# Kernel optimization log

Measured on AMD Instinct MI355X. Metric: run time of the kernel, lower is better.

The kernel has to match this reference:

```python
import jax, jax.numpy as jnp
import numpy as np

H = 128  # hidden_dim
F = 64   # node_feat_dim


def setup_inputs() -> dict:
    key = jax.random.key(0)
    ks = jax.random.split(key, 24)
    N, E, NR, NT = 50000, 400000, 20000, 20000
    inp = {
        "mol_x": jax.random.normal(ks[0], (N, F), jnp.float32),
        "pos": jax.random.normal(ks[1], (N, 3), jnp.float32),
        "reaction_x": jax.random.normal(ks[2], (NR, F), jnp.float32),
        "target_x": jax.random.normal(ks[3], (NT, F), jnp.float32),
        "edge_index": jax.random.randint(ks[4], (2, E), 0, N, jnp.int32),
    }
    def lin(k, fan_in, fan_out):
        s = 1.0 / np.sqrt(fan_in)
        kw, kb = jax.random.split(k)
        W = jax.random.uniform(kw, (fan_in, fan_out), jnp.float32, -s, s)
        b = jax.random.uniform(kb, (fan_out,), jnp.float32, -s, s)
        return W, b
    inp["W_node"], inp["b_node"] = lin(ks[5], F, H)
    inp["W_att1"], inp["b_att1"] = lin(ks[6], 2 * H + 3, H)
    inp["W_att2"], inp["b_att2"] = lin(ks[7], H, 1)
    inp["W_upd"], inp["b_upd"] = lin(ks[8], H, H)
    inp["Wy1"], inp["by1"] = lin(ks[9], H, 64)
    inp["Wy2"], inp["by2"] = lin(ks[10], 64, 1)
    inp["Wa1"], inp["ba1"] = lin(ks[11], H, 64)
    inp["Wa2"], inp["ba2"] = lin(ks[12], 64, 1)
    return inp


def reference(mol_x, pos, reaction_x, target_x, edge_index,
              W_node, b_node, W_att1, b_att1, W_att2, b_att2,
              W_upd, b_upd, Wy1, by1, Wy2, by2, Wa1, ba1, Wa2, ba2):
    N = mol_x.shape[0]
    # node encoder
    h = mol_x @ W_node + b_node                      # [N, H]
    src, dst = edge_index[0], edge_index[1]          # PyG: x_j = source, x_i = target
    x_j = h[src]                                      # [E, H]
    x_i = h[dst]                                      # [E, H]
    dist = pos[dst] - pos[src]                        # [E, 3]
    cat = jnp.concatenate([x_i, x_j, dist], axis=1)   # [E, 2H+3]
    s = jax.nn.relu(cat @ W_att1 + b_att1) @ W_att2 + b_att2  # [E, 1]
    att = jax.nn.softmax(s, axis=0)                   # global softmax over edges (dim=0)
    msg = x_j * att                                   # [E, H]
    aggr = jax.ops.segment_sum(msg, dst, num_segments=N)  # scatter-add -> [N, H]
    mol_feats = aggr @ W_upd + b_upd                  # [N, H]
    # heads on reaction / target graphs
    rh = reaction_x @ W_node + b_node
    th = target_x @ W_node + b_node
    pred_yield = (jax.nn.relu(rh @ Wy1 + by1) @ Wy2 + by2).squeeze(-1)
    pred_activity = (jax.nn.relu(th @ Wa1 + ba1) @ Wa2 + ba2).squeeze(-1)
    return pred_yield, pred_activity, mol_feats
```

## Files before the change

### kernel.cpp

```cpp
#include <hip/hip_runtime.h>
#include <hip/hip_bf16.h>

typedef unsigned short ushort_t;
typedef __attribute__((ext_vector_type(8))) short s16x8;
typedef __attribute__((ext_vector_type(4))) float f32x4;

__device__ inline unsigned short f2bf(float x) {
    unsigned u = __float_as_uint(x);
    return (unsigned short)((u + 0x7FFFu + ((u >> 16) & 1u)) >> 16);
}
__device__ inline float bflo(unsigned u) { return __uint_as_float(u << 16); }
__device__ inline float bfhi(unsigned u) { return __uint_as_float(u & 0xffff0000u); }

__device__ inline void pack_one(const float* __restrict__ W, int K, int N,
                                ushort_t* __restrict__ dst, int g) {
    int KT = K / 32;
    int nt = g / (KT * 64);
    int rem = g % (KT * 64);
    int kt = rem / 64, lane = rem % 64;
    int n = nt * 16 + (lane & 15);
    int kbase = kt * 32 + ((lane >> 4) << 3);
    ushort_t tmp[8];
#pragma unroll
    for (int j = 0; j < 8; ++j) tmp[j] = f2bf(W[(size_t)(kbase + j) * N + n]);
    uint4 pk;
    pk.x = tmp[0] | ((unsigned)tmp[1] << 16);
    pk.y = tmp[2] | ((unsigned)tmp[3] << 16);
    pk.z = tmp[4] | ((unsigned)tmp[5] << 16);
    pk.w = tmp[6] | ((unsigned)tmp[7] << 16);
    *(uint4*)&dst[(size_t)g * 8] = pk;
}

__global__ void convert_w(const float* __restrict__ Wn, const float* __restrict__ W1,
                          const float* __restrict__ Wu, const float* __restrict__ Wy1,
                          const float* __restrict__ Wa1,
                          ushort_t* __restrict__ Wnb, ushort_t* __restrict__ W1tb,
                          ushort_t* __restrict__ W1mb, ushort_t* __restrict__ Wub,
                          ushort_t* __restrict__ Wy1b, ushort_t* __restrict__ Wa1b,
                          int* __restrict__ counts8, int N) {
    int t = blockIdx.x * 256 + threadIdx.x;
    if (t < 1024)       pack_one(Wn, 64, 128, Wnb, t);
    else if (t < 3072)  pack_one(W1, 128, 128, W1tb, t - 1024);
    else if (t < 5120)  pack_one(W1 + 128 * 128, 128, 128, W1mb, t - 3072);
    else if (t < 7168)  pack_one(Wu, 128, 128, Wub, t - 5120);
    else if (t < 8192)  pack_one(Wy1, 128, 64, Wy1b, t - 7168);
    else if (t < 9216)  pack_one(Wa1, 128, 64, Wa1b, t - 8192);
    int stride = gridDim.x * 256;
    for (int i = t; i < 8 * N; i += stride) counts8[i] = 0;
}

__global__ void encode_pq(const float* __restrict__ x, const ushort_t* __restrict__ Wnb,
                          const float* __restrict__ bn, const ushort_t* __restrict__ W1tb,
                          const ushort_t* __restrict__ W1mb, const float* __restrict__ b1,
                          const float* __restrict__ Wd, const float* __restrict__ pos,
                          ushort_t* __restrict__ hb, ushort_t* __restrict__ P,
                          ushort_t* __restrict__ Q, const int* __restrict__ dst,
                          int* __restrict__ counts8, int nrows, int E) {
    __shared__ ushort_t ldsH[16 * 136];
    __shared__ float ldsWd[384];
    int t = threadIdx.x;
    for (int i = t; i < 384; i += 256) ldsWd[i] = Wd[i];
    int w = t >> 6, lane = t & 63;
    int c = lane & 15, q = lane >> 4;
    int r0 = blockIdx.x * 16;
    int rowA = r0 + c; if (rowA >= nrows) rowA = nrows - 1;

    s16x8 xa[2];
#pragma unroll
    for (int kt = 0; kt < 2; ++kt) {
        const float* xp = &x[(size_t)rowA * 64 + kt * 32 + q * 8];
        float4 v0 = *(const float4*)xp;
        float4 v1 = *(const float4*)(xp + 4);
        s16x8 a;
        a[0] = (short)f2bf(v0.x); a[1] = (short)f2bf(v0.y);
        a[2] = (short)f2bf(v0.z); a[3] = (short)f2bf(v0.w);
        a[4] = (short)f2bf(v1.x); a[5] = (short)f2bf(v1.y);
        a[6] = (short)f2bf(v1.z); a[7] = (short)f2bf(v1.w);
        xa[kt] = a;
    }
#pragma unroll
    for (int half = 0; half < 2; ++half) {
        int nt = w + half * 4;
        f32x4 acc = {0.f, 0.f, 0.f, 0.f};
#pragma unroll
        for (int kt = 0; kt < 2; ++kt) {
            s16x8 b = *(const s16x8*)&Wnb[((nt * 2 + kt) * 64 + lane) * 8];
            acc = __builtin_amdgcn_mfma_f32_16x16x32_bf16(xa[kt], b, acc, 0, 0, 0);
        }
        float bi = bn[nt * 16 + c];
#pragma unroll
        for (int r = 0; r < 4; ++r) {
            int row = r0 + q * 4 + r;
            ushort_t hv = f2bf(acc[r] + bi);
            ldsH[(q * 4 + r) * 136 + nt * 16 + c] = hv;
            if (row < nrows) hb[(size_t)row * 128 + nt * 16 + c] = hv;
        }
    }
    __syncthreads();
    s16x8 ha[4];
#pragma unroll
    for (int kt = 0; kt < 4; ++kt)
        ha[kt] = *(const s16x8*)&ldsH[c * 136 + kt * 32 + q * 8];
    float prx[4], pry[4], prz[4];
#pragma unroll
    for (int r = 0; r < 4; ++r) {
        int row = r0 + q * 4 + r;
        int rowc = (row < nrows) ? row : (nrows - 1);
        prx[r] = pos[rowc * 3];
        pry[r] = pos[rowc * 3 + 1];
        prz[r] = pos[rowc * 3 + 2];
    }
#pragma unroll
    for (int half = 0; half < 2; ++half) {
        int nt = w + half * 4;
        f32x4 pa = {0.f, 0.f, 0.f, 0.f}, qa = pa;
#pragma unroll
        for (int kt = 0; kt < 4; ++kt) {
            s16x8 bp = *(const s16x8*)&W1tb[((nt * 4 + kt) * 64 + lane) * 8];
            s16x8 bq = *(const s16x8*)&W1mb[((nt * 4 + kt) * 64 + lane) * 8];
            pa = __builtin_amdgcn_mfma_f32_16x16x32_bf16(ha[kt], bp, pa, 0, 0, 0);
            qa = __builtin_amdgcn_mfma_f32_16x16x32_bf16(ha[kt], bq, qa, 0, 0, 0);
        }
        int col = nt * 16 + c;
        float bi = b1[col];
        float wd0 = ldsWd[col], wd1 = ldsWd[128 + col], wd2 = ldsWd[256 + col];
#pragma unroll
        for (int r = 0; r < 4; ++r) {
            int row = r0 + q * 4 + r;
            if (row < nrows) {
                float pd = prx[r] * wd0 + pry[r] * wd1 + prz[r] * wd2;
                P[(size_t)row * 128 + col] = f2bf(pa[r] + bi + pd);
                Q[(size_t)row * 128 + col] = f2bf(qa[r] - pd);
            }
        }
    }
    int* myc = counts8 + (size_t)(blockIdx.x & 7) * nrows;
    for (int e = blockIdx.x * 256 + t; e < E; e += gridDim.x * 256)
        atomicAdd(&myc[dst[e]], 1);
}

__global__ void scan1(const int* __restrict__ counts8, int* __restrict__ counts,
                      int* __restrict__ offs, int* __restrict__ partials, int N) {
    __shared__ int sm[256];
    int i = blockIdx.x * 256 + threadIdx.x;
    int v = 0;
    if (i < N) {
#pragma unroll
        for (int j = 0; j < 8; ++j) v += counts8[(size_t)j * N + i];
        counts[i] = v;
    }
    sm[threadIdx.x] = v; __syncthreads();
    for (int off = 1; off < 256; off <<= 1) {
        int add = (threadIdx.x >= off) ? sm[threadIdx.x - off] : 0;
        __syncthreads();
        sm[threadIdx.x] += add;
        __syncthreads();
    }
    if (i < N) offs[i] = sm[threadIdx.x] - v;
    if (threadIdx.x == 255) partials[blockIdx.x] = sm[255];
}

__global__ void scan_add(int* __restrict__ offs, int* __restrict__ cursor,
                         const int* __restrict__ partials, int nb, int N) {
    __shared__ int sm[256];
    int t = threadIdx.x;
    sm[t] = (t < nb && t < blockIdx.x) ? partials[t] : 0;
    __syncthreads();
    for (int off = 128; off > 0; off >>= 1) {
        if (t < off) sm[t] += sm[t + off];
        __syncthreads();
    }
    int basev = sm[0];
    int i = blockIdx.x * 256 + t;
    if (i < N) {
        int v = offs[i] + basev;
        offs[i] = v;
        cursor[i] = v;
    }
}

__global__ void scatter_edges(const int* __restrict__ src, const int* __restrict__ dst,
                              int* __restrict__ cursor, int2* __restrict__ csr, int E) {
    int e = blockIdx.x * 256 + threadIdx.x;
    if (e < E) {
        int s = src[e], d = dst[e];
        int p = atomicAdd(&cursor[d], 1);
        csr[p] = make_int2(s, d);
    }
}

__global__ __launch_bounds__(256, 4)
void edge_score(const ushort_t* __restrict__ P, const ushort_t* __restrict__ Q,
                const float* __restrict__ W2, const float* __restrict__ b2,
                int2* __restrict__ csr,
                float* __restrict__ redm, float* __restrict__ rede, int E) {
    __shared__ float wsh[128];
    __shared__ float smm[4], sme[4];
    int t = threadIdx.x;
    if (t < 128) wsh[t] = W2[t];
    __syncthreads();
    int w = t >> 6, lane = t & 63;
    int g = lane >> 4, c = lane & 15;
    float wv[8];
#pragma unroll
    for (int j = 0; j < 8; ++j) wv[j] = wsh[c * 8 + j];
    float b2v = b2[0];
    int base = blockIdx.x * 128 + w * 32;
    float m = -1e30f, ev = 0.f;
#pragma unroll
    for (int ch = 0; ch < 2; ++ch) {
        int sa[4], da[4];
        uint4 pr[4], qr[4];
#pragma unroll
        for (int it = 0; it < 4; ++it) {
            int p = base + ch * 16 + it * 4 + g;
            int pp = (p < E) ? p : (E - 1);
            int2 v = csr[pp];
            sa[it] = v.x; da[it] = v.y;
        }
#pragma unroll
        for (int it = 0; it < 4; ++it)
            qr[it] = *(const uint4*)&Q[(size_t)sa[it] * 128 + c * 8];
#pragma unroll
        for (int it = 0; it < 4; ++it)
            pr[it] = *(const uint4*)&P[(size_t)da[it] * 128 + c * 8];
#pragma unroll
        for (int it = 0; it < 4; ++it) {
            unsigned pw[4] = {pr[it].x, pr[it].y, pr[it].z, pr[it].w};
            unsigned qw[4] = {qr[it].x, qr[it].y, qr[it].z, qr[it].w};
            float v = 0.f;
#pragma unroll
            for (int jj = 0; jj < 4; ++jj) {
                float pe = bflo(pw[jj]) + bflo(qw[jj]);
                float po = bfhi(pw[jj]) + bfhi(qw[jj]);
                v += fmaxf(pe, 0.f) * wv[2 * jj] + fmaxf(po, 0.f) * wv[2 * jj + 1];
            }
#pragma unroll
            for (int off = 1; off < 16; off <<= 1) v += __shfl_xor(v, off, 64);
            int p = base + ch * 16 + it * 4 + g;
            if (c == 0 && p < E) {
                float sv = v + b2v;
                csr[p] = make_int2(sa[it], __float_as_int(sv));
                float nm = fmaxf(m, sv);
                ev = ev * __expf(m - nm) + __expf(sv - nm);
                m = nm;
            }
        }
    }
#pragma unroll
    for (int off = 1; off < 64; off <<= 1) {
        float m2 = __shfl_xor(m, off, 64);
        float e2 = __shfl_xor(ev, off, 64);
        float M = fmaxf(m, m2);
        ev = ev * __expf(m - M) + e2 * __expf(m2 - M);
        m = M;
    }
    if (lane == 0) { smm[w] = m; sme[w] = ev; }
    __syncthreads();
    if (t == 0) {
        float m01 = fmaxf(smm[0], smm[1]), m23 = fmaxf(smm[2], smm[3]);
        float M = fmaxf(m01, m23);
        float z = sme[0] * __expf(smm[0] - M) + sme[1] * __expf(smm[1] - M)
                + sme[2] * __expf(smm[2] - M) + sme[3] * __expf(smm[3] - M);
        redm[blockIdx.x] = M;
        rede[blockIdx.x] = z;
    }
}

__global__ void reduce_partials(const float* __restrict__ redm,
                                const float* __restrict__ rede,
                                float* __restrict__ gmz, int nbE) {
    __shared__ float smm[256], sme[256];
    int t = threadIdx.x;
    float m = -1e30f, z = 0.f;
    for (int i = t; i < nbE; i += 256) {
        float m2 = redm[i], z2 = rede[i];
        float M = fmaxf(m, m2);
        z = z * __expf(m - M) + z2 * __expf(m2 - M);
        m = M;
    }
    smm[t] = m; sme[t] = z; __syncthreads();
    for (int off = 128; off > 0; off >>= 1) {
        if (t < off) {
            float m1 = smm[t], m2 = smm[t + off];
            float e1 = sme[t], e2 = sme[t + off];
            float M = fmaxf(m1, m2);
            smm[t] = M;
            sme[t] = e1 * __expf(m1 - M) + e2 * __expf(m2 - M);
        }
        __syncthreads();
    }
    if (t == 0) { gmz[0] = smm[0]; gmz[1] = 1.f / sme[0]; }
}

__global__ void gather_head(const ushort_t* __restrict__ hb, const int2* __restrict__ csr,
                            const int* __restrict__ offs, const int* __restrict__ deg,
                            const float* __restrict__ gmz,
                            const ushort_t* __restrict__ Wub, const float* __restrict__ bu,
                            float* __restrict__ molf, int N, int nbG,
                            const float* __restrict__ rx, const float* __restrict__ tx,
                            const ushort_t* __restrict__ Wnb, const float* __restrict__ bn,
                            const ushort_t* __restrict__ Wy1b, const float* __restrict__ by1,
                            const float* __restrict__ Wy2, const float* __restrict__ by2,
                            const ushort_t* __restrict__ Wa1b, const float* __restrict__ ba1,
                            const float* __restrict__ Wa2, const float* __restrict__ ba2,
                            float* __restrict__ out, int nb1, int NR, int NT) {
    int t = threadIdx.x;
    int w = t >> 6, lane = t & 63;
    int c = lane & 15, q = lane >> 4;

    if (blockIdx.x < nbG) {
        __shared__ ushort_t ldsA[16 * 136];
        float gm = gmz[0], inv = gmz[1];

        int g = lane >> 4;
        int r0 = blockIdx.x * 16;
#pragma unroll
        for (int i = 0; i < 4; ++i) {
            int node = r0 + w * 4 + i;
            float a[8] = {0.f, 0.f, 0.f, 0.f, 0.f, 0.f, 0.f, 0.f};
            if (node < N) {
                int start = offs[node], d = deg[node];
                int k = g;
                for (; k + 4 < d; k += 8) {
                    int2 v0 = csr[start + k];
                    int2 v1 = csr[start + k + 4];
                    uint4 h0 = *(const uint4*)&hb[(size_t)v0.x * 128 + c * 8];
                    uint4 h1 = *(const uint4*)&hb[(size_t)v1.x * 128 + c * 8];
                    float at0 = __expf(__int_as_float(v0.y) - gm) * inv;
                    float at1 = __expf(__int_as_float(v1.y) - gm) * inv;
                    a[0] += bflo(h0.x) * at0; a[1] += bfhi(h0.x) * at0;
                    a[2] += bflo(h0.y) * at0; a[3] += bfhi(h0.y) * at0;
                    a[4] += bflo(h0.z) * at0; a[5] += bfhi(h0.z) * at0;
                    a[6] += bflo(h0.w) * at0; a[7] += bfhi(h0.w) * at0;
                    a[0] += bflo(h1.x) * at1; a[1] += bfhi(h1.x) * at1;
                    a[2] += bflo(h1.y) * at1; a[3] += bfhi(h1.y) * at1;
                    a[4] += bflo(h1.z) * at1; a[5] += bfhi(h1.z) * at1;
                    a[6] += bflo(h1.w) * at1; a[7] += bfhi(h1.w) * at1;
                }
                if (k < d) {
                    int2 v0 = csr[start + k];
                    uint4 h0 = *(const uint4*)&hb[(size_t)v0.x * 128 + c * 8];
                    float at0 = __expf(__int_as_float(v0.y) - gm) * inv;
                    a[0] += bflo(h0.x) * at0; a[1] += bfhi(h0.x) * at0;
                    a[2] += bflo(h0.y) * at0; a[3] += bfhi(h0.y) * at0;
                    a[4] += bflo(h0.z) * at0; a[5] += bfhi(h0.z) * at0;
                    a[6] += bflo(h0.w) * at0; a[7] += bfhi(h0.w) * at0;
                }
            }
#pragma unroll
            for (int j = 0; j < 8; ++j) {
                a[j] += __shfl_xor(a[j], 16, 64);
                a[j] += __shfl_xor(a[j], 32, 64);
            }
            if (g == 0) {
                uint4 pk;
                pk.x = f2bf(a[0]) | ((unsigned)f2bf(a[1]) << 16);
                pk.y = f2bf(a[2]) | ((unsigned)f2bf(a[3]) << 16);
                pk.z = f2bf(a[4]) | ((unsigned)f2bf(a[5]) << 16);
                pk.w = f2bf(a[6]) | ((unsigned)f2bf(a[7]) << 16);
                *(uint4*)&ldsA[(w * 4 + i) * 136 + c * 8] = pk;
            }
        }
        __syncthreads();
        int ntA = w, ntB = w + 4;
        f32x4 acc0 = {0.f, 0.f, 0.f, 0.f}, acc1 = acc0;
#pragma unroll
        for (int kt = 0; kt < 4; ++kt) {
            s16x8 av = *(const s16x8*)&ldsA[c * 136 + kt * 32 + q * 8];
            s16x8 b0 = *(const s16x8*)&Wub[((ntA * 4 + kt) * 64 + lane) * 8];
            s16x8 b1 = *(const s16x8*)&Wub[((ntB * 4 + kt) * 64 + lane) * 8];
            acc0 = __builtin_amdgcn_mfma_f32_16x16x32_bf16(av, b0, acc0, 0, 0, 0);
            acc1 = __builtin_amdgcn_mfma_f32_16x16x32_bf16(av, b1, acc1, 0, 0, 0);
        }
        float bi0 = bu[ntA * 16 + c], bi1 = bu[ntB * 16 + c];
#pragma unroll
        for (int r = 0; r < 4; ++r) {
            int row = r0 + q * 4 + r;
            if (row < N) {
                molf[(size_t)row * 128 + ntA * 16 + c] = acc0[r] + bi0;
                molf[(size_t)row * 128 + ntB * 16 + c] = acc1[r] + bi1;
            }
        }
    } else {
        __shared__ ushort_t ldsX[16 * 72];
        __shared__ ushort_t ldsB[16 * 136];
        __shared__ float part[64];
        int blk = blockIdx.x - nbG;
        const float* x; const ushort_t* W1b; const float* b1; const float* W2; const float* b2;
        float* o; int r0, nrows;
        if (blk < nb1) { x = rx; W1b = Wy1b; b1 = by1; W2 = Wy2; b2 = by2; o = out; r0 = blk * 16; nrows = NR; }
        else { x = tx; W1b = Wa1b; b1 = ba1; W2 = Wa2; b2 = ba2; o = out + NR; r0 = (blk - nb1) * 16; nrows = NT; }
        {
            int row = t >> 4, c4 = (t & 15) * 4;
            float4 v = *(const float4*)&x[(size_t)(r0 + row) * 64 + c4];
            uint2 pk;
            pk.x = f2bf(v.x) | ((unsigned)f2bf(v.y) << 16);
            pk.y = f2bf(v.z) | ((unsigned)f2bf(v.w) << 16);
            *(uint2*)&ldsX[row * 72 + c4] = pk;
        }
        __syncthreads();
        {
            int ntA = w, ntB = w + 4;
            f32x4 acc0 = {0.f, 0.f, 0.f, 0.f}, acc1 = acc0;
#pragma unroll
            for (int kt = 0; kt < 2; ++kt) {
                s16x8 a = *(const s16x8*)&ldsX[c * 72 + kt * 32 + q * 8];
                s16x8 b0 = *(const s16x8*)&Wnb[((ntA * 2 + kt) * 64 + lane) * 8];
                s16x8 b1v = *(const s16x8*)&Wnb[((ntB * 2 + kt) * 64 + lane) * 8];
                acc0 = __builtin_amdgcn_mfma_f32_16x16x32_bf16(a, b0, acc0, 0, 0, 0);
                acc1 = __builtin_amdgcn_mfma_f32_16x16x32_bf16(a, b1v, acc1, 0, 0, 0);
            }
            float bi0 = bn[ntA * 16 + c], bi1 = bn[ntB * 16 + c];
#pragma unroll
            for (int r = 0; r < 4; ++r) {
                int row = q * 4 + r;
                ldsB[row * 136 + ntA * 16 + c] = f2bf(acc0[r] + bi0);
                ldsB[row * 136 + ntB * 16 + c] = f2bf(acc1[r] + bi1);
            }
        }
        __syncthreads();
        {
            f32x4 acc = {0.f, 0.f, 0.f, 0.f};
#pragma unroll
            for (int kt = 0; kt < 4; ++kt) {
                s16x8 a = *(const s16x8*)&ldsB[c * 136 + kt * 32 + q * 8];
                s16x8 b0 = *(const s16x8*)&W1b[((w * 4 + kt) * 64 + lane) * 8];
                acc = __builtin_amdgcn_mfma_f32_16x16x32_bf16(a, b0, acc, 0, 0, 0);
            }
            float bi = b1[w * 16 + c], w2v = W2[w * 16 + c];
#pragma unroll
            for (int r = 0; r < 4; ++r) {
                float u = fmaxf(acc[r] + bi, 0.f) * w2v;
#pragma unroll
                for (int mm = 1; mm < 16; mm <<= 1) u += __shfl_xor(u, mm, 64);
                if (c == 0) part[w * 16 + q * 4 + r] = u;
            }
        }
        __syncthreads();
        if (t < 16) {
            int row = r0 + t;
            if (row < nrows)
                o[row] = part[t] + part[16 + t] + part[32 + t] + part[48 + t] + b2[0];
        }
    }
}

extern "C" void kernel_launch(void* const* d_in, const int* in_sizes, int n_in,
                              void* d_out, int out_size, void* d_ws, size_t ws_size,
                              hipStream_t stream) {
    const float* mol_x      = (const float*)d_in[0];
    const float* pos        = (const float*)d_in[1];
    const float* reaction_x = (const float*)d_in[2];
    const float* target_x   = (const float*)d_in[3];
    const int*   ei         = (const int*)d_in[4];
    const float* W_node = (const float*)d_in[5];
    const float* b_node = (const float*)d_in[6];
    const float* W_att1 = (const float*)d_in[7];
    const float* b_att1 = (const float*)d_in[8];
    const float* W_att2 = (const float*)d_in[9];
    const float* b_att2 = (const float*)d_in[10];
    const float* W_upd  = (const float*)d_in[11];
    const float* b_upd  = (const float*)d_in[12];
    const float* Wy1 = (const float*)d_in[13];
    const float* by1 = (const float*)d_in[14];
    const float* Wy2 = (const float*)d_in[15];
    const float* by2 = (const float*)d_in[16];
    const float* Wa1 = (const float*)d_in[17];
    const float* ba1 = (const float*)d_in[18];
    const float* Wa2 = (const float*)d_in[19];
    const float* ba2 = (const float*)d_in[20];

    int N  = in_sizes[0] / 64;
    int E  = in_sizes[4] / 2;
    int NR = in_sizes[2] / 64;
    int NT = in_sizes[3] / 64;

    float* out = (float*)d_out;

    int nbE = (E + 127) / 128;
    int nbG = (N + 15) / 16;
    int nbH = (NR + NT) / 16;

    char* wp = (char*)d_ws;
    ushort_t* hb = (ushort_t*)wp;  wp += (size_t)N * 128 * 2;
    ushort_t* Qb = (ushort_t*)wp;  wp += (size_t)N * 128 * 2;
    float* redm  = (float*)wp;     wp += (size_t)nbE * 4;
    float* rede  = (float*)wp;     wp += (size_t)nbE * 4;
    float* gmz   = (float*)wp;     wp += 2 * 4;
    int* counts8 = (int*)wp;       wp += (size_t)8 * N * 4;
    int* counts  = (int*)wp;       wp += (size_t)N * 4;
    int* offs    = (int*)wp;       wp += (size_t)N * 4;
    int* cursor  = (int*)wp;       wp += (size_t)N * 4;
    int* partials= (int*)wp;       wp += 256 * 4;
    int2* csr    = (int2*)wp;      wp += (size_t)E * 8;
    ushort_t* Wnb  = (ushort_t*)wp; wp += 8192 * 2;
    ushort_t* W1tb = (ushort_t*)wp; wp += 16384 * 2;
    ushort_t* W1mb = (ushort_t*)wp; wp += 16384 * 2;
    ushort_t* Wub  = (ushort_t*)wp; wp += 16384 * 2;
    ushort_t* Wy1b = (ushort_t*)wp; wp += 8192 * 2;
    ushort_t* Wa1b = (ushort_t*)wp; wp += 8192 * 2;
    ushort_t* Pb = (ushort_t*)(out + NR + NT);
    float* molf  = out + NR + NT;

    const int* srcp = ei;
    const int* dstp = ei + E;
    int nbN = (N + 255) / 256;
    int nbS = (E + 255) / 256;

    convert_w<<<nbN, 256, 0, stream>>>(W_node, W_att1, W_upd, Wy1, Wa1,
                                       Wnb, W1tb, W1mb, Wub, Wy1b, Wa1b, counts8, N);
    encode_pq<<<(N + 15) / 16, 256, 0, stream>>>(mol_x, Wnb, b_node, W1tb, W1mb, b_att1,
                                                 W_att1 + 256 * 128, pos,
                                                 hb, Pb, Qb, dstp, counts8, N, E);
    scan1<<<nbN, 256, 0, stream>>>(counts8, counts, offs, partials, N);
    scan_add<<<nbN, 256, 0, stream>>>(offs, cursor, partials, nbN, N);
    scatter_edges<<<nbS, 256, 0, stream>>>(srcp, dstp, cursor, csr, E);
    edge_score<<<nbE, 256, 0, stream>>>(Pb, Qb, W_att2, b_att2,
                                        csr, redm, rede, E);
    reduce_partials<<<1, 256, 0, stream>>>(redm, rede, gmz, nbE);
    gather_head<<<nbG + nbH, 256, 0, stream>>>(hb, csr, offs, counts, gmz,
                                               Wub, b_upd, molf, N, nbG,
                                               reaction_x, target_x, Wnb, b_node,
                                               Wy1b, by1, Wy2, by2, Wa1b, ba1, Wa2, ba2,
                                               out, NR / 16, NR, NT);
}
```

Measured before the change: 226.7 us.

## Fuse edge scoring with weighted aggregation using unnormalized exp and atomic node sums

Edge scoring now aggregates exp(score)*h[src] per destination on the fly, using segmented accumulation over the dst-sorted CSR, plain stores for interior segments and atomics at boundaries, plus a global atomic sum for the normalizer. This drops the softmax max-reduction kernel and the separate gather pass, so scores are no longer written back and CSR/hb are not reread. The node update then scales the fp32 accumulator by 1/Z. The cost is a large fp32 accumulator that must be zeroed and atomics on it. Skipping max subtraction risks exp overflow for large scores. Interior-segment plain stores assume no other thread touches those nodes, which holds only because edges are sorted by dst.

```diff
diff --git a/kernel.cpp b/kernel.cpp
--- a/kernel.cpp
+++ b/kernel.cpp
@@ -37,7 +37,8 @@
                           ushort_t* __restrict__ Wnb, ushort_t* __restrict__ W1tb,
                           ushort_t* __restrict__ W1mb, ushort_t* __restrict__ Wub,
                           ushort_t* __restrict__ Wy1b, ushort_t* __restrict__ Wa1b,
-                          int* __restrict__ counts8, int N) {
+                          int* __restrict__ counts8, float* __restrict__ U,
+                          float* __restrict__ Zg, int N) {
     int t = blockIdx.x * 256 + threadIdx.x;
     if (t < 1024)       pack_one(Wn, 64, 128, Wnb, t);
     else if (t < 3072)  pack_one(W1, 128, 128, W1tb, t - 1024);
@@ -47,6 +48,10 @@
     else if (t < 9216)  pack_one(Wa1, 128, 64, Wa1b, t - 8192);
     int stride = gridDim.x * 256;
     for (int i = t; i < 8 * N; i += stride) counts8[i] = 0;
+    float4 z4 = {0.f, 0.f, 0.f, 0.f};
+    float4* U4 = (float4*)U;
+    for (int i = t; i < 32 * N; i += stride) U4[i] = z4;
+    if (t == 0) Zg[0] = 0.f;
 }
 
 __global__ void encode_pq(const float* __restrict__ x, const ushort_t* __restrict__ Wnb,
@@ -139,15 +144,14 @@
         atomicAdd(&myc[dst[e]], 1);
 }
 
-__global__ void scan1(const int* __restrict__ counts8, int* __restrict__ counts,
-                      int* __restrict__ offs, int* __restrict__ partials, int N) {
+__global__ void scan1(const int* __restrict__ counts8, int* __restrict__ offs,
+                      int* __restrict__ partials, int N) {
     __shared__ int sm[256];
     int i = blockIdx.x * 256 + threadIdx.x;
     int v = 0;
     if (i < N) {
 #pragma unroll
         for (int j = 0; j < 8; ++j) v += counts8[(size_t)j * N + i];
-        counts[i] = v;
     }
     sm[threadIdx.x] = v; __syncthreads();
     for (int off = 1; off < 256; off <<= 1) {
@@ -190,12 +194,13 @@
 }
 
 __global__ __launch_bounds__(256, 4)
-void edge_score(const ushort_t* __restrict__ P, const ushort_t* __restrict__ Q,
+void edge_fused(const ushort_t* __restrict__ P, const ushort_t* __restrict__ Q,
+                const ushort_t* __restrict__ hb,
                 const float* __restrict__ W2, const float* __restrict__ b2,
-                int2* __restrict__ csr,
-                float* __restrict__ redm, float* __restrict__ rede, int E) {
+                const int2* __restrict__ csr,
+                float* __restrict__ U, float* __restrict__ Zg, int E) {
     __shared__ float wsh[128];
-    __shared__ float smm[4], sme[4];
+    __shared__ float zsh[4];
     int t = threadIdx.x;
     if (t < 128) wsh[t] = W2[t];
     __syncthreads();
@@ -205,27 +210,31 @@
 #pragma unroll
     for (int j = 0; j < 8; ++j) wv[j] = wsh[c * 8 + j];
     float b2v = b2[0];
-    int base = blockIdx.x * 128 + w * 32;
-    float m = -1e30f, ev = 0.f;
-#pragma unroll
-    for (int ch = 0; ch < 2; ++ch) {
+    int base = blockIdx.x * 512 + w * 128 + g * 32;
+    float acc[8] = {0.f, 0.f, 0.f, 0.f, 0.f, 0.f, 0.f, 0.f};
+    float zacc = 0.f;
+    int cur = -1, first_dst = -1;
+    bool done = false;
+    for (int bt = 0; bt < 8 && !done; ++bt) {
         int sa[4], da[4];
-        uint4 pr[4], qr[4];
+        uint4 qr[4], hr[4], pr[4];
 #pragma unroll
         for (int it = 0; it < 4; ++it) {
-            int p = base + ch * 16 + it * 4 + g;
+            int p = base + bt * 4 + it;
             int pp = (p < E) ? p : (E - 1);
             int2 v = csr[pp];
             sa[it] = v.x; da[it] = v.y;
         }
 #pragma unroll
-        for (int it = 0; it < 4; ++it)
+        for (int it = 0; it < 4; ++it) {
             qr[it] = *(const uint4*)&Q[(size_t)sa[it] * 128 + c * 8];
-#pragma unroll
-        for (int it = 0; it < 4; ++it)
+            hr[it] = *(const uint4*)&hb[(size_t)sa[it] * 128 + c * 8];
             pr[it] = *(const uint4*)&P[(size_t)da[it] * 128 + c * 8];
+        }
 #pragma unroll
         for (int it = 0; it < 4; ++it) {
+            int p = base + bt * 4 + it;
+            if (p >= E) { done = true; break; }
             unsigned pw[4] = {pr[it].x, pr[it].y, pr[it].z, pr[it].w};
             unsigned qw[4] = {qr[it].x, qr[it].y, qr[it].z, qr[it].w};
             float v = 0.f;
@@ -237,130 +246,78 @@
             }
 #pragma unroll
             for (int off = 1; off < 16; off <<= 1) v += __shfl_xor(v, off, 64);
-            int p = base + ch * 16 + it * 4 + g;
-            if (c == 0 && p < E) {
-                float sv = v + b2v;
-                csr[p] = make_int2(sa[it], __float_as_int(sv));
-                float nm = fmaxf(m, sv);
-                ev = ev * __expf(m - nm) + __expf(sv - nm);
-                m = nm;
-            }
-        }
-    }
-#pragma unroll
-    for (int off = 1; off < 64; off <<= 1) {
-        float m2 = __shfl_xor(m, off, 64);
-        float e2 = __shfl_xor(ev, off, 64);
-        float M = fmaxf(m, m2);
-        ev = ev * __expf(m - M) + e2 * __expf(m2 - M);
-        m = M;
-    }
-    if (lane == 0) { smm[w] = m; sme[w] = ev; }
+            float ev = __expf(v + b2v);
+            if (da[it] != cur) {
+                if (cur >= 0) {
+                    float* up = &U[(size_t)cur * 128 + c * 8];
+                    if (cur == first_dst) {
+#pragma unroll
+                        for (int j = 0; j < 8; ++j) atomicAdd(&up[j], acc[j]);
+                    } else {
+                        float4 a0 = {acc[0], acc[1], acc[2], acc[3]};
+                        float4 a1 = {acc[4], acc[5], acc[6], acc[7]};
+                        *(float4*)up = a0;
+                        *(float4*)(up + 4) = a1;
+                    }
+#pragma unroll
+                    for (int j = 0; j < 8; ++j) acc[j] = 0.f;
+                }
+                if (cur < 0) first_dst = da[it];
+                cur = da[it];
+            }
+            unsigned hw[4] = {hr[it].x, hr[it].y, hr[it].z, hr[it].w};
+            acc[0] += bflo(hw[0]) * ev; acc[1] += bfhi(hw[0]) * ev;
+            acc[2] += bflo(hw[1]) * ev; acc[3] += bfhi(hw[1]) * ev;
+            acc[4] += bflo(hw[2]) * ev; acc[5] += bfhi(hw[2]) * ev;
+            acc[6] += bflo(hw[3]) * ev; acc[7] += bfhi(hw[3]) * ev;
+            zacc += ev;
+        }
+    }
+    if (cur >= 0) {
+        float* up = &U[(size_t)cur * 128 + c * 8];
+#pragma unroll
+        for (int j = 0; j < 8; ++j) atomicAdd(&up[j], acc[j]);
+    }
+    float zv = (c == 0) ? zacc : 0.f;
+#pragma unroll
+    for (int off = 1; off < 64; off <<= 1) zv += __shfl_xor(zv, off, 64);
+    if (lane == 0) zsh[w] = zv;
     __syncthreads();
-    if (t == 0) {
-        float m01 = fmaxf(smm[0], smm[1]), m23 = fmaxf(smm[2], smm[3]);
-        float M = fmaxf(m01, m23);
-        float z = sme[0] * __expf(smm[0] - M) + sme[1] * __expf(smm[1] - M)
-                + sme[2] * __expf(smm[2] - M) + sme[3] * __expf(smm[3] - M);
-        redm[blockIdx.x] = M;
-        rede[blockIdx.x] = z;
-    }
-}
-
-__global__ void reduce_partials(const float* __restrict__ redm,
-                                const float* __restrict__ rede,
-                                float* __restrict__ gmz, int nbE) {
-    __shared__ float smm[256], sme[256];
-    int t = threadIdx.x;
-    float m = -1e30f, z = 0.f;
-    for (int i = t; i < nbE; i += 256) {
-        float m2 = redm[i], z2 = rede[i];
-        float M = fmaxf(m, m2);
-        z = z * __expf(m - M) + z2 * __expf(m2 - M);
-        m = M;
-    }
-    smm[t] = m; sme[t] = z; __syncthreads();
-    for (int off = 128; off > 0; off >>= 1) {
-        if (t < off) {
-            float m1 = smm[t], m2 = smm[t + off];
-            float e1 = sme[t], e2 = sme[t + off];
-            float M = fmaxf(m1, m2);
-            smm[t] = M;
-            sme[t] = e1 * __expf(m1 - M) + e2 * __expf(m2 - M);
-        }
-        __syncthreads();
-    }
-    if (t == 0) { gmz[0] = smm[0]; gmz[1] = 1.f / sme[0]; }
-}
-
-__global__ void gather_head(const ushort_t* __restrict__ hb, const int2* __restrict__ csr,
-                            const int* __restrict__ offs, const int* __restrict__ deg,
-                            const float* __restrict__ gmz,
-                            const ushort_t* __restrict__ Wub, const float* __restrict__ bu,
-                            float* __restrict__ molf, int N, int nbG,
-                            const float* __restrict__ rx, const float* __restrict__ tx,
-                            const ushort_t* __restrict__ Wnb, const float* __restrict__ bn,
-                            const ushort_t* __restrict__ Wy1b, const float* __restrict__ by1,
-                            const float* __restrict__ Wy2, const float* __restrict__ by2,
-                            const ushort_t* __restrict__ Wa1b, const float* __restrict__ ba1,
-                            const float* __restrict__ Wa2, const float* __restrict__ ba2,
-                            float* __restrict__ out, int nb1, int NR, int NT) {
+    if (t == 0) atomicAdd(Zg, zsh[0] + zsh[1] + zsh[2] + zsh[3]);
+}
+
+__global__ void node_upd(const float* __restrict__ U, const float* __restrict__ Zg,
+                         const ushort_t* __restrict__ Wub, const float* __restrict__ bu,
+                         float* __restrict__ molf, int N, int nbG,
+                         const float* __restrict__ rx, const float* __restrict__ tx,
+                         const ushort_t* __restrict__ Wnb, const float* __restrict__ bn,
+                         const ushort_t* __restrict__ Wy1b, const float* __restrict__ by1,
+                         const float* __restrict__ Wy2, const float* __restrict__ by2,
+                         const ushort_t* __restrict__ Wa1b, const float* __restrict__ ba1,
+                         const float* __restrict__ Wa2, const float* __restrict__ ba2,
+                         float* __restrict__ out, int nb1, int NR, int NT) {
     int t = threadIdx.x;
     int w = t >> 6, lane = t & 63;
     int c = lane & 15, q = lane >> 4;
 
     if (blockIdx.x < nbG) {
         __shared__ ushort_t ldsA[16 * 136];
-        float gm = gmz[0], inv = gmz[1];
-
-        int g = lane >> 4;
+        float inv = 1.f / Zg[0];
         int r0 = blockIdx.x * 16;
-#pragma unroll
-        for (int i = 0; i < 4; ++i) {
-            int node = r0 + w * 4 + i;
-            float a[8] = {0.f, 0.f, 0.f, 0.f, 0.f, 0.f, 0.f, 0.f};
-            if (node < N) {
-                int start = offs[node], d = deg[node];
-                int k = g;
-                for (; k + 4 < d; k += 8) {
-                    int2 v0 = csr[start + k];
-                    int2 v1 = csr[start + k + 4];
-                    uint4 h0 = *(const uint4*)&hb[(size_t)v0.x * 128 + c * 8];
-                    uint4 h1 = *(const uint4*)&hb[(size_t)v1.x * 128 + c * 8];
-                    float at0 = __expf(__int_as_float(v0.y) - gm) * inv;
-                    float at1 = __expf(__int_as_float(v1.y) - gm) * inv;
-                    a[0] += bflo(h0.x) * at0; a[1] += bfhi(h0.x) * at0;
-                    a[2] += bflo(h0.y) * at0; a[3] += bfhi(h0.y) * at0;
-                    a[4] += bflo(h0.z) * at0; a[5] += bfhi(h0.z) * at0;
-                    a[6] += bflo(h0.w) * at0; a[7] += bfhi(h0.w) * at0;
-                    a[0] += bflo(h1.x) * at1; a[1] += bfhi(h1.x) * at1;
-                    a[2] += bflo(h1.y) * at1; a[3] += bfhi(h1.y) * at1;
-                    a[4] += bflo(h1.z) * at1; a[5] += bfhi(h1.z) * at1;
-                    a[6] += bflo(h1.w) * at1; a[7] += bfhi(h1.w) * at1;
-                }
-                if (k < d) {
-                    int2 v0 = csr[start + k];
-                    uint4 h0 = *(const uint4*)&hb[(size_t)v0.x * 128 + c * 8];
-                    float at0 = __expf(__int_as_float(v0.y) - gm) * inv;
-                    a[0] += bflo(h0.x) * at0; a[1] += bfhi(h0.x) * at0;
-                    a[2] += bflo(h0.y) * at0; a[3] += bfhi(h0.y) * at0;
-                    a[4] += bflo(h0.z) * at0; a[5] += bfhi(h0.z) * at0;
-                    a[6] += bflo(h0.w) * at0; a[7] += bfhi(h0.w) * at0;
-                }
-            }
-#pragma unroll
-            for (int j = 0; j < 8; ++j) {
-                a[j] += __shfl_xor(a[j], 16, 64);
-                a[j] += __shfl_xor(a[j], 32, 64);
-            }
-            if (g == 0) {
-                uint4 pk;
-                pk.x = f2bf(a[0]) | ((unsigned)f2bf(a[1]) << 16);
-                pk.y = f2bf(a[2]) | ((unsigned)f2bf(a[3]) << 16);
-                pk.z = f2bf(a[4]) | ((unsigned)f2bf(a[5]) << 16);
-                pk.w = f2bf(a[6]) | ((unsigned)f2bf(a[7]) << 16);
-                *(uint4*)&ldsA[(w * 4 + i) * 136 + c * 8] = pk;
-            }
+        {
+            int idx = t * 8;
+            int row = idx >> 7;
+            int col = idx & 127;
+            int rr = r0 + row; if (rr >= N) rr = N - 1;
+            const float* up = &U[(size_t)rr * 128 + col];
+            float4 a = *(const float4*)up;
+            float4 b = *(const float4*)(up + 4);
+            uint4 pk;
+            pk.x = f2bf(a.x * inv) | ((unsigned)f2bf(a.y * inv) << 16);
+            pk.y = f2bf(a.z * inv) | ((unsigned)f2bf(a.w * inv) << 16);
+            pk.z = f2bf(b.x * inv) | ((unsigned)f2bf(b.y * inv) << 16);
+            pk.w = f2bf(b.z * inv) | ((unsigned)f2bf(b.w * inv) << 16);
+            *(uint4*)&ldsA[row * 136 + col] = pk;
         }
         __syncthreads();
         int ntA = w, ntB = w + 4;
@@ -478,18 +435,16 @@
 
     float* out = (float*)d_out;
 
-    int nbE = (E + 127) / 128;
     int nbG = (N + 15) / 16;
     int nbH = (NR + NT) / 16;
+    int nbB = (E + 511) / 512;
 
     char* wp = (char*)d_ws;
     ushort_t* hb = (ushort_t*)wp;  wp += (size_t)N * 128 * 2;
     ushort_t* Qb = (ushort_t*)wp;  wp += (size_t)N * 128 * 2;
-    float* redm  = (float*)wp;     wp += (size_t)nbE * 4;
-    float* rede  = (float*)wp;     wp += (size_t)nbE * 4;
-    float* gmz   = (float*)wp;     wp += 2 * 4;
+    float* U     = (float*)wp;     wp += (size_t)N * 128 * 4;
+    float* Zg    = (float*)wp;     wp += 256;
     int* counts8 = (int*)wp;       wp += (size_t)8 * N * 4;
-    int* counts  = (int*)wp;       wp += (size_t)N * 4;
     int* offs    = (int*)wp;       wp += (size_t)N * 4;
     int* cursor  = (int*)wp;       wp += (size_t)N * 4;
     int* partials= (int*)wp;       wp += 256 * 4;
@@ -507,21 +462,21 @@
     const int* dstp = ei + E;
     int nbN = (N + 255) / 256;
     int nbS = (E + 255) / 256;
-
-    convert_w<<<nbN, 256, 0, stream>>>(W_node, W_att1, W_upd, Wy1, Wa1,
-                                       Wnb, W1tb, W1mb, Wub, Wy1b, Wa1b, counts8, N);
+    int nbC = 784;
+
+    convert_w<<<nbC, 256, 0, stream>>>(W_node, W_att1, W_upd, Wy1, Wa1,
+                                       Wnb, W1tb, W1mb, Wub, Wy1b, Wa1b,
+                                       counts8, U, Zg, N);
     encode_pq<<<(N + 15) / 16, 256, 0, stream>>>(mol_x, Wnb, b_node, W1tb, W1mb, b_att1,
                                                  W_att1 + 256 * 128, pos,
                                                  hb, Pb, Qb, dstp, counts8, N, E);
-    scan1<<<nbN, 256, 0, stream>>>(counts8, counts, offs, partials, N);
+    scan1<<<nbN, 256, 0, stream>>>(counts8, offs, partials, N);
     scan_add<<<nbN, 256, 0, stream>>>(offs, cursor, partials, nbN, N);
     scatter_edges<<<nbS, 256, 0, stream>>>(srcp, dstp, cursor, csr, E);
-    edge_score<<<nbE, 256, 0, stream>>>(Pb, Qb, W_att2, b_att2,
-                                        csr, redm, rede, E);
-    reduce_partials<<<1, 256, 0, stream>>>(redm, rede, gmz, nbE);
-    gather_head<<<nbG + nbH, 256, 0, stream>>>(hb, csr, offs, counts, gmz,
-                                               Wub, b_upd, molf, N, nbG,
-                                               reaction_x, target_x, Wnb, b_node,
-                                               Wy1b, by1, Wy2, by2, Wa1b, ba1, Wa2, ba2,
-                                               out, NR / 16, NR, NT);
-}
+    edge_fused<<<nbB, 256, 0, stream>>>(Pb, Qb, hb, W_att2, b_att2,
+                                        csr, U, Zg, E);
+    node_upd<<<nbG + nbH, 256, 0, stream>>>(U, Zg, Wub, b_upd, molf, N, nbG,
+                                            reaction_x, target_x, Wnb, b_node,
+                                            Wy1b, by1, Wy2, by2, Wa1b, ba1, Wa2, ba2,
+                                            out, NR / 16, NR, NT);
+}
```

After: 309.3 us. 36.4% more time.
